# Optimization experiments

Measured on AMD Instinct MI355X. Metric: run time of the kernel, lower is better.

## Reference

```python
import jax, jax.numpy as jnp
import numpy as np

N_NODES = 50000
N_EDGES = 800000
D_IN = 128
D_OUT = 128


def setup_inputs() -> dict:
    key = jax.random.key(0)
    k_x, k_r, k_c, k_v, k_w = jax.random.split(key, 5)
    x = jax.random.normal(k_x, (N_NODES, D_IN), dtype=jnp.float32)
    edge_row = jax.random.randint(k_r, (N_EDGES,), 0, N_NODES)  # destination nodes
    edge_col = jax.random.randint(k_c, (N_EDGES,), 0, N_NODES)  # source nodes
    edge_val = jax.random.uniform(k_v, (N_EDGES,), dtype=jnp.float32)
    W = jax.random.normal(k_w, (D_OUT, D_IN), dtype=jnp.float32) * (1.0 / np.sqrt(D_IN))
    bias = jnp.zeros((D_OUT,), dtype=jnp.float32)
    return {"x": x, "edge_row": edge_row, "edge_col": edge_col,
            "edge_val": edge_val, "W": W, "bias": bias}


def reference(x, edge_row, edge_col, edge_val, W, bias):
    # support = linear(x)   (nn.Linear with bias=False: x @ W.T)
    support = jnp.einsum('ni,oi->no', x, W)  # [N, D_OUT]
    # out = sparse.mm(adj, support): gather source rows, scale by edge value,
    # scatter-add into destination rows.
    msgs = edge_val[:, None] * support[edge_col]  # [E, D_OUT]
    out = jax.ops.segment_sum(msgs, edge_row, num_segments=N_NODES)
    return out + bias
```

## Files before the change

### kernel.cpp

```cpp
#include <hip/hip_runtime.h>
#include <hip/hip_bf16.h>


constexpr int D     = 128;
constexpr int NPB   = 64;
constexpr int CAP   = 2048;
constexpr int C1    = 3200;
constexpr int BT    = 1024;
constexpr int NBMAX = 1024;

__device__ inline unsigned int bf1(float f) {
    unsigned int u = __float_as_uint(f);
    return (u + 0x7fffu + ((u >> 16) & 1u)) >> 16;
}
__device__ inline unsigned int bf2(float lo, float hi) {
    return bf1(lo) | (bf1(hi) << 16);
}
__device__ inline unsigned int cvt2(float a, float b) {
    __hip_bfloat162 h = __float22bfloat162_rn(float2{a, b});
    return *reinterpret_cast<unsigned int*>(&h);
}
__device__ inline float bflo(unsigned int u) { return __uint_as_float(u << 16); }
__device__ inline float bfhi(unsigned int u) { return __uint_as_float(u & 0xffff0000u); }

__global__ __launch_bounds__(256) void cvt_bf16_kernel(const float* __restrict__ in,
                                                       uint4* __restrict__ out, int n8,
                                                       int* __restrict__ gcursor, int nb) {
    int i = blockIdx.x * 256 + threadIdx.x;
    if (i < nb) gcursor[i] = 0;
    if (i >= n8) return;
    const float4* p = (const float4*)in + (size_t)i * 2;
    float4 a = p[0], b = p[1];
    uint4 r;
    r.x = cvt2(a.x, a.y); r.y = cvt2(a.z, a.w);
    r.z = cvt2(b.x, b.y); r.w = cvt2(b.z, b.w);
    out[i] = r;
}

__global__ __launch_bounds__(256) void gemm_mfma_kernel(const float* __restrict__ x,
                                                        const unsigned short* __restrict__ Wb,
                                                        unsigned short* __restrict__ supb,
                                                        int n_nodes) {
    using frag  = __attribute__((ext_vector_type(8))) short;
    using f32x4 = __attribute__((ext_vector_type(4))) float;
    union FU { uint4 u; frag f; };
    const int wv = threadIdx.x >> 6;
    const int lane = threadIdx.x & 63;
    const int m = lane & 15, quad = lane >> 4;
    const int row0 = blockIdx.x * 128 + wv * 32;
    const int r0 = min(row0 + m, n_nodes - 1);
    const int r1 = min(row0 + 16 + m, n_nodes - 1);

    frag a0[4], a1[4];
#pragma unroll
    for (int kf = 0; kf < 4; ++kf) {
        const float4* xp0 = (const float4*)(x + (size_t)r0 * D + kf * 32 + quad * 8);
        float4 p = xp0[0], q = xp0[1];
        FU t;
        t.u.x = cvt2(p.x, p.y); t.u.y = cvt2(p.z, p.w);
        t.u.z = cvt2(q.x, q.y); t.u.w = cvt2(q.z, q.w);
        a0[kf] = t.f;
        const float4* xp1 = (const float4*)(x + (size_t)r1 * D + kf * 32 + quad * 8);
        p = xp1[0]; q = xp1[1];
        t.u.x = cvt2(p.x, p.y); t.u.y = cvt2(p.z, p.w);
        t.u.z = cvt2(q.x, q.y); t.u.w = cvt2(q.z, q.w);
        a1[kf] = t.f;
    }

    f32x4 acc0[8], acc1[8];
#pragma unroll
    for (int ct = 0; ct < 8; ++ct) {
        acc0[ct] = (f32x4){0.f, 0.f, 0.f, 0.f};
        acc1[ct] = (f32x4){0.f, 0.f, 0.f, 0.f};
    }

#pragma unroll
    for (int ct = 0; ct < 8; ++ct) {
        const unsigned short* wrow = Wb + (size_t)(ct * 16 + m) * D;
#pragma unroll
        for (int kf = 0; kf < 4; ++kf) {
            frag b = *(const frag*)(wrow + kf * 32 + quad * 8);
            acc0[ct] = __builtin_amdgcn_mfma_f32_16x16x32_bf16(a0[kf], b, acc0[ct], 0, 0, 0);
            acc1[ct] = __builtin_amdgcn_mfma_f32_16x16x32_bf16(a1[kf], b, acc1[ct], 0, 0, 0);
        }
    }

#pragma unroll
    for (int ct = 0; ct < 8; ++ct) {
#pragma unroll
        for (int r = 0; r < 4; ++r) {
            int rr0 = row0 + quad * 4 + r;
            if (rr0 < n_nodes)
                supb[(size_t)rr0 * D + ct * 16 + m] = (unsigned short)bf1(acc0[ct][r]);
            int rr1 = row0 + 16 + quad * 4 + r;
            if (rr1 < n_nodes)
                supb[(size_t)rr1 * D + ct * 16 + m] = (unsigned short)bf1(acc1[ct][r]);
        }
    }
}

__global__ __launch_bounds__(BT) void binpass_kernel(const int* __restrict__ erow,
                                                     const int* __restrict__ ecol,
                                                     const float* __restrict__ eval,
                                                     int* __restrict__ gcursor,
                                                     int2* __restrict__ coarse,
                                                     int n_edges, int nb) {
    __shared__ int bkcnt[NBMAX];
    __shared__ int bkoff[NBMAX];
    __shared__ int wsum[16];
    __shared__ int gbase[NBMAX];
    __shared__ unsigned short slotbk[C1];
    __shared__ int2 stage[C1];
    const int t = threadIdx.x;
    const int base = blockIdx.x * C1;
    const int m = min(C1, n_edges - base);

    for (int i = t; i < nb; i += BT) bkcnt[i] = 0;
    __syncthreads();

    constexpr int EPT = (C1 + BT - 1) / BT;
    int  bk[EPT], rank[EPT];
    int2 pk[EPT];
#pragma unroll
    for (int j = 0; j < EPT; ++j) {
        int i = t + j * BT;
        bk[j] = -1;
        if (i < m) {
            int e = base + i;
            int dst = erow[e];
            int b = dst / NPB;
            bk[j] = b;
            rank[j] = atomicAdd(&bkcnt[b], 1);
            pk[j] = make_int2(ecol[e] | ((dst & (NPB - 1)) << 20),
                              __float_as_int(eval[e]));
        }
    }
    __syncthreads();

    {
        const int w = t >> 6, l = t & 63;
        int v = (t < nb) ? bkcnt[t] : 0;
        int inc = v;
#pragma unroll
        for (int o = 1; o < 64; o <<= 1) {
            int u = __shfl_up(inc, o, 64);
            if (l >= o) inc += u;
        }
        if (l == 63) wsum[w] = inc;
        __syncthreads();
        if (t < 16) {
            int wv2 = wsum[t];
            int winc = wv2;
#pragma unroll
            for (int o = 1; o < 16; o <<= 1) {
                int u = __shfl_up(winc, o, 16);
                if (t >= o) winc += u;
            }
            wsum[t] = winc - wv2;
        }
        __syncthreads();
        if (t < nb) bkoff[t] = inc - v + wsum[w];
    }
    __syncthreads();

#pragma unroll
    for (int j = 0; j < EPT; ++j) {
        if (bk[j] >= 0) {
            int s = bkoff[bk[j]] + rank[j];
            stage[s] = pk[j];
            slotbk[s] = (unsigned short)bk[j];
        }
    }
    if (t < nb) {
        int c = bkcnt[t];
        gbase[t] = (c > 0) ? (t * CAP + atomicAdd(&gcursor[t], c)) : 0;
    }
    __syncthreads();

    for (int i = t; i < m; i += BT) {
        int b = slotbk[i];
        int p = gbase[b] + (i - bkoff[b]);
        if (p < (b + 1) * CAP) coarse[p] = stage[i];
    }
}

__global__ __launch_bounds__(BT) void sortgather_kernel(const int* __restrict__ gcursor,
                                                        const int2* __restrict__ coarse,
                                                        const unsigned short* __restrict__ supb,
                                                        const float* __restrict__ bias,
                                                        float* __restrict__ out,
                                                        int n_nodes) {
    __shared__ int ncnt[NPB];
    __shared__ int noff[NPB];
    __shared__ int ncur[NPB];
    __shared__ int2 sorted[CAP];
    const int t = threadIdx.x;
    const int b = blockIdx.x;
    const int node0 = b * NPB;
    const int m = min(gcursor[b], CAP);
    const int2* src = coarse + (size_t)b * CAP;

    if (t < NPB) ncnt[t] = 0;
    __syncthreads();

    for (int i = t; i < m; i += BT)
        atomicAdd(&ncnt[(src[i].x >> 20) & (NPB - 1)], 1);
    __syncthreads();

    if (t < NPB) {
        int v = ncnt[t];
        int inc = v;
        for (int o = 1; o < NPB; o <<= 1) {
            int u = __shfl_up(inc, o, 64);
            if (t >= o) inc += u;
        }
        noff[t] = inc - v;
        ncur[t] = inc - v;
    }
    __syncthreads();

    for (int i = t; i < m; i += BT) {
        int2 e = src[i];
        int dl = (e.x >> 20) & (NPB - 1);
        int p = atomicAdd(&ncur[dl], 1);
        sorted[p] = make_int2(e.x & 0xFFFFF, e.y);
    }
    __syncthreads();

    const int qw = t >> 4;
    const int l16 = t & 15;
    const int node = node0 + qw;
    if (node >= n_nodes) return;
    const int beg = noff[qw];
    const int end = beg + ncnt[qw];

    const float4* b4 = (const float4*)(bias + l16 * 8);
    float4 acc0 = b4[0], acc1 = b4[1];

    int e = beg;
    for (; e + 1 < end; e += 2) {
        int2 d0 = sorted[e], d1 = sorted[e + 1];
        uint4 u0 = *(const uint4*)(supb + (size_t)d0.x * D + l16 * 8);
        uint4 u1 = *(const uint4*)(supb + (size_t)d1.x * D + l16 * 8);
        float v0 = __int_as_float(d0.y), v1 = __int_as_float(d1.y);
        acc0.x += v0 * bflo(u0.x) + v1 * bflo(u1.x);
        acc0.y += v0 * bfhi(u0.x) + v1 * bfhi(u1.x);
        acc0.z += v0 * bflo(u0.y) + v1 * bflo(u1.y);
        acc0.w += v0 * bfhi(u0.y) + v1 * bfhi(u1.y);
        acc1.x += v0 * bflo(u0.z) + v1 * bflo(u1.z);
        acc1.y += v0 * bfhi(u0.z) + v1 * bfhi(u1.z);
        acc1.z += v0 * bflo(u0.w) + v1 * bflo(u1.w);
        acc1.w += v0 * bfhi(u0.w) + v1 * bfhi(u1.w);
    }
    if (e < end) {
        int2 d0 = sorted[e];
        uint4 u0 = *(const uint4*)(supb + (size_t)d0.x * D + l16 * 8);
        float v0 = __int_as_float(d0.y);
        acc0.x += v0 * bflo(u0.x); acc0.y += v0 * bfhi(u0.x);
        acc0.z += v0 * bflo(u0.y); acc0.w += v0 * bfhi(u0.y);
        acc1.x += v0 * bflo(u0.z); acc1.y += v0 * bfhi(u0.z);
        acc1.z += v0 * bflo(u0.w); acc1.w += v0 * bfhi(u0.w);
    }
    float4* o4 = (float4*)(out + (size_t)node * D + l16 * 8);
    o4[0] = acc0;
    o4[1] = acc1;
}

__global__ __launch_bounds__(256) void init_out_kernel(float4* __restrict__ out4,
                                                       const float4* __restrict__ bias4,
                                                       int total4) {
    int i = blockIdx.x * 256 + threadIdx.x;
    if (i < total4) out4[i] = bias4[i & 31];
}

__global__ __launch_bounds__(256) void scatter_fb_kernel(const int* __restrict__ erow,
                                                         const int* __restrict__ ecol,
                                                         const float* __restrict__ eval,
                                                         const unsigned short* __restrict__ supb,
                                                         float* __restrict__ out,
                                                         int n_edges) {
    int e = blockIdx.x * 8 + (threadIdx.x >> 5);
    if (e >= n_edges) return;
    int lane = threadIdx.x & 31;
    int src = ecol[e], dst = erow[e];
    float v = eval[e];
    const unsigned short* sp = supb + (size_t)src * D + lane * 4;
    float* op = out + (size_t)dst * D + lane * 4;
#pragma unroll
    for (int j = 0; j < 4; ++j)
        atomicAdd(op + j, v * __uint_as_float(((unsigned)sp[j]) << 16));
}

static inline size_t align_up(size_t v, size_t a) { return (v + a - 1) & ~(a - 1); }

extern "C" void kernel_launch(void* const* d_in, const int* in_sizes, int n_in,
                              void* d_out, int out_size, void* d_ws, size_t ws_size,
                              hipStream_t stream) {
    const float* x    = (const float*)d_in[0];
    const int*   erow = (const int*)d_in[1];
    const int*   ecol = (const int*)d_in[2];
    const float* eval = (const float*)d_in[3];
    const float* W    = (const float*)d_in[4];
    const float* bias = (const float*)d_in[5];
    float* out = (float*)d_out;

    const int n_nodes = in_sizes[0] / D;
    const int n_edges = in_sizes[1];
    const int nb = (n_nodes + NPB - 1) / NPB;

    char* base = (char*)d_ws;
    size_t off = 0;
    unsigned short* supb = (unsigned short*)(base + off); off = align_up(off + (size_t)n_nodes * D * 2, 256);
    unsigned short* Wb   = (unsigned short*)(base + off); off = align_up(off + (size_t)D * D * 2, 256);
    int*  gcursor = (int*)(base + off);  off = align_up(off + (size_t)nb * 4, 256);
    int2* coarse  = (int2*)(base + off); off = align_up(off + (size_t)nb * CAP * 8, 256);

    const int n8 = D * D / 8;
    const int cvt_grid = (max(n8, nb) + 255) / 256;
    const bool fast = (n_nodes < (1 << 20)) && (nb <= NBMAX) && (off <= ws_size);

    cvt_bf16_kernel<<<cvt_grid, 256, 0, stream>>>(W, (uint4*)Wb, n8, gcursor, fast ? nb : 0);
    gemm_mfma_kernel<<<(n_nodes + 127) / 128, 256, 0, stream>>>(x, Wb, supb, n_nodes);

    if (fast) {
        binpass_kernel<<<(n_edges + C1 - 1) / C1, BT, 0, stream>>>(
            erow, ecol, eval, gcursor, coarse, n_edges, nb);
        sortgather_kernel<<<nb, BT, 0, stream>>>(
            gcursor, coarse, supb, bias, out, n_nodes);
    } else {
        int total4 = n_nodes * (D / 4);
        init_out_kernel<<<(total4 + 255) / 256, 256, 0, stream>>>(
            (float4*)out, (const float4*)bias, total4);
        scatter_fb_kernel<<<(n_edges + 7) / 8, 256, 0, stream>>>(
            erow, ecol, eval, supb, out, n_edges);
    }
}
```

Before: 144.7 us.

## Fuse GEMM and edge binning into one heterogeneous kernel launch

```diff
diff --git a/kernel.cpp b/kernel.cpp
--- a/kernel.cpp
+++ b/kernel.cpp
@@ -5,7 +5,7 @@
 constexpr int D     = 128;
 constexpr int NPB   = 64;
 constexpr int CAP   = 2048;
-constexpr int C1    = 3200;
+constexpr int C1    = 2048;
 constexpr int BT    = 1024;
 constexpr int NBMAX = 1024;
 
@@ -13,9 +13,6 @@
     unsigned int u = __float_as_uint(f);
     return (u + 0x7fffu + ((u >> 16) & 1u)) >> 16;
 }
-__device__ inline unsigned int bf2(float lo, float hi) {
-    return bf1(lo) | (bf1(hi) << 16);
-}
 __device__ inline unsigned int cvt2(float a, float b) {
     __hip_bfloat162 h = __float22bfloat162_rn(float2{a, b});
     return *reinterpret_cast<unsigned int*>(&h);
@@ -23,164 +20,160 @@
 __device__ inline float bflo(unsigned int u) { return __uint_as_float(u << 16); }
 __device__ inline float bfhi(unsigned int u) { return __uint_as_float(u & 0xffff0000u); }
 
-__global__ __launch_bounds__(256) void cvt_bf16_kernel(const float* __restrict__ in,
-                                                       uint4* __restrict__ out, int n8,
-                                                       int* __restrict__ gcursor, int nb) {
-    int i = blockIdx.x * 256 + threadIdx.x;
-    if (i < nb) gcursor[i] = 0;
-    if (i >= n8) return;
-    const float4* p = (const float4*)in + (size_t)i * 2;
-    float4 a = p[0], b = p[1];
-    uint4 r;
-    r.x = cvt2(a.x, a.y); r.y = cvt2(a.z, a.w);
-    r.z = cvt2(b.x, b.y); r.w = cvt2(b.z, b.w);
-    out[i] = r;
-}
-
-__global__ __launch_bounds__(256) void gemm_mfma_kernel(const float* __restrict__ x,
-                                                        const unsigned short* __restrict__ Wb,
-                                                        unsigned short* __restrict__ supb,
-                                                        int n_nodes) {
-    using frag  = __attribute__((ext_vector_type(8))) short;
-    using f32x4 = __attribute__((ext_vector_type(4))) float;
-    union FU { uint4 u; frag f; };
-    const int wv = threadIdx.x >> 6;
-    const int lane = threadIdx.x & 63;
-    const int m = lane & 15, quad = lane >> 4;
-    const int row0 = blockIdx.x * 128 + wv * 32;
-    const int r0 = min(row0 + m, n_nodes - 1);
-    const int r1 = min(row0 + 16 + m, n_nodes - 1);
-
-    frag a0[4], a1[4];
-#pragma unroll
-    for (int kf = 0; kf < 4; ++kf) {
-        const float4* xp0 = (const float4*)(x + (size_t)r0 * D + kf * 32 + quad * 8);
-        float4 p = xp0[0], q = xp0[1];
-        FU t;
-        t.u.x = cvt2(p.x, p.y); t.u.y = cvt2(p.z, p.w);
-        t.u.z = cvt2(q.x, q.y); t.u.w = cvt2(q.z, q.w);
-        a0[kf] = t.f;
-        const float4* xp1 = (const float4*)(x + (size_t)r1 * D + kf * 32 + quad * 8);
-        p = xp1[0]; q = xp1[1];
-        t.u.x = cvt2(p.x, p.y); t.u.y = cvt2(p.z, p.w);
-        t.u.z = cvt2(q.x, q.y); t.u.w = cvt2(q.z, q.w);
-        a1[kf] = t.f;
-    }
-
-    f32x4 acc0[8], acc1[8];
-#pragma unroll
-    for (int ct = 0; ct < 8; ++ct) {
-        acc0[ct] = (f32x4){0.f, 0.f, 0.f, 0.f};
-        acc1[ct] = (f32x4){0.f, 0.f, 0.f, 0.f};
-    }
-
-#pragma unroll
-    for (int ct = 0; ct < 8; ++ct) {
-        const unsigned short* wrow = Wb + (size_t)(ct * 16 + m) * D;
+__global__ __launch_bounds__(256) void fused_gemm_bin_kernel(
+        const float* __restrict__ x, const float* __restrict__ W,
+        const int* __restrict__ erow, const int* __restrict__ ecol,
+        const float* __restrict__ eval,
+        int* __restrict__ gcursor, int2* __restrict__ coarse,
+        unsigned short* __restrict__ supb,
+        int n_edges, int nb, int n_nodes, int bin_blocks) {
+    if ((int)blockIdx.x < bin_blocks) {
+        __shared__ int bkcnt[NBMAX];
+        __shared__ int bkoff[NBMAX];
+        __shared__ int wsum[4];
+        __shared__ int gbase[NBMAX];
+        __shared__ unsigned short slotbk[C1];
+        __shared__ int2 stage[C1];
+        const int t = threadIdx.x;
+        const int base = blockIdx.x * C1;
+        const int m = min(C1, n_edges - base);
+
+        for (int i = t; i < NBMAX; i += 256) bkcnt[i] = 0;
+        __syncthreads();
+
+        constexpr int EPT = C1 / 256;
+        int  bk[EPT], rank[EPT];
+        int2 pk[EPT];
+#pragma unroll
+        for (int j = 0; j < EPT; ++j) {
+            int i = t + j * 256;
+            bk[j] = -1;
+            if (i < m) {
+                int e = base + i;
+                int dst = erow[e];
+                int b = dst / NPB;
+                bk[j] = b;
+                rank[j] = atomicAdd(&bkcnt[b], 1);
+                pk[j] = make_int2(ecol[e] | ((dst & (NPB - 1)) << 20),
+                                  __float_as_int(eval[e]));
+            }
+        }
+        __syncthreads();
+
+        {
+            const int w = t >> 6, l = t & 63;
+            const int b0 = 4 * t;
+            int c0 = bkcnt[b0], c1 = bkcnt[b0 + 1];
+            int c2 = bkcnt[b0 + 2], c3 = bkcnt[b0 + 3];
+            int s = c0 + c1 + c2 + c3;
+            int inc = s;
+#pragma unroll
+            for (int o = 1; o < 64; o <<= 1) {
+                int u = __shfl_up(inc, o, 64);
+                if (l >= o) inc += u;
+            }
+            if (l == 63) wsum[w] = inc;
+            __syncthreads();
+            if (t < 4) {
+                int v = wsum[t];
+                int winc = v;
+#pragma unroll
+                for (int o = 1; o < 4; o <<= 1) {
+                    int u = __shfl_up(winc, o, 4);
+                    if (t >= o) winc += u;
+                }
+                wsum[t] = winc - v;
+            }
+            __syncthreads();
+            int p = inc - s + wsum[w];
+            bkoff[b0]     = p;
+            bkoff[b0 + 1] = p + c0;
+            bkoff[b0 + 2] = p + c0 + c1;
+            bkoff[b0 + 3] = p + c0 + c1 + c2;
+        }
+        __syncthreads();
+
+#pragma unroll
+        for (int j = 0; j < EPT; ++j) {
+            if (bk[j] >= 0) {
+                int s2 = bkoff[bk[j]] + rank[j];
+                stage[s2] = pk[j];
+                slotbk[s2] = (unsigned short)bk[j];
+            }
+        }
+        for (int i = t; i < nb; i += 256) {
+            int c = bkcnt[i];
+            gbase[i] = (c > 0) ? (i * CAP + atomicAdd(&gcursor[i], c)) : 0;
+        }
+        __syncthreads();
+
+        for (int i = t; i < m; i += 256) {
+            int b = slotbk[i];
+            int p = gbase[b] + (i - bkoff[b]);
+            if (p < (b + 1) * CAP) coarse[p] = stage[i];
+        }
+    } else {
+        using frag  = __attribute__((ext_vector_type(8))) short;
+        using f32x4 = __attribute__((ext_vector_type(4))) float;
+        union FU { uint4 u; frag f; };
+        const int wv = threadIdx.x >> 6;
+        const int lane = threadIdx.x & 63;
+        const int mm = lane & 15, quad = lane >> 4;
+        const int row0 = (blockIdx.x - bin_blocks) * 128 + wv * 32;
+        const int r0 = min(row0 + mm, n_nodes - 1);
+        const int r1 = min(row0 + 16 + mm, n_nodes - 1);
+
+        frag a0[4], a1[4];
 #pragma unroll
         for (int kf = 0; kf < 4; ++kf) {
-            frag b = *(const frag*)(wrow + kf * 32 + quad * 8);
-            acc0[ct] = __builtin_amdgcn_mfma_f32_16x16x32_bf16(a0[kf], b, acc0[ct], 0, 0, 0);
-            acc1[ct] = __builtin_amdgcn_mfma_f32_16x16x32_bf16(a1[kf], b, acc1[ct], 0, 0, 0);
-        }
-    }
-
-#pragma unroll
-    for (int ct = 0; ct < 8; ++ct) {
-#pragma unroll
-        for (int r = 0; r < 4; ++r) {
-            int rr0 = row0 + quad * 4 + r;
-            if (rr0 < n_nodes)
-                supb[(size_t)rr0 * D + ct * 16 + m] = (unsigned short)bf1(acc0[ct][r]);
-            int rr1 = row0 + 16 + quad * 4 + r;
-            if (rr1 < n_nodes)
-                supb[(size_t)rr1 * D + ct * 16 + m] = (unsigned short)bf1(acc1[ct][r]);
-        }
-    }
-}
-
-__global__ __launch_bounds__(BT) void binpass_kernel(const int* __restrict__ erow,
-                                                     const int* __restrict__ ecol,
-                                                     const float* __restrict__ eval,
-                                                     int* __restrict__ gcursor,
-                                                     int2* __restrict__ coarse,
-                                                     int n_edges, int nb) {
-    __shared__ int bkcnt[NBMAX];
-    __shared__ int bkoff[NBMAX];
-    __shared__ int wsum[16];
-    __shared__ int gbase[NBMAX];
-    __shared__ unsigned short slotbk[C1];
-    __shared__ int2 stage[C1];
-    const int t = threadIdx.x;
-    const int base = blockIdx.x * C1;
-    const int m = min(C1, n_edges - base);
-
-    for (int i = t; i < nb; i += BT) bkcnt[i] = 0;
-    __syncthreads();
-
-    constexpr int EPT = (C1 + BT - 1) / BT;
-    int  bk[EPT], rank[EPT];
-    int2 pk[EPT];
-#pragma unroll
-    for (int j = 0; j < EPT; ++j) {
-        int i = t + j * BT;
-        bk[j] = -1;
-        if (i < m) {
-            int e = base + i;
-            int dst = erow[e];
-            int b = dst / NPB;
-            bk[j] = b;
-            rank[j] = atomicAdd(&bkcnt[b], 1);
-            pk[j] = make_int2(ecol[e] | ((dst & (NPB - 1)) << 20),
-                              __float_as_int(eval[e]));
-        }
-    }
-    __syncthreads();
-
-    {
-        const int w = t >> 6, l = t & 63;
-        int v = (t < nb) ? bkcnt[t] : 0;
-        int inc = v;
-#pragma unroll
-        for (int o = 1; o < 64; o <<= 1) {
-            int u = __shfl_up(inc, o, 64);
-            if (l >= o) inc += u;
-        }
-        if (l == 63) wsum[w] = inc;
-        __syncthreads();
-        if (t < 16) {
-            int wv2 = wsum[t];
-            int winc = wv2;
-#pragma unroll
-            for (int o = 1; o < 16; o <<= 1) {
-                int u = __shfl_up(winc, o, 16);
-                if (t >= o) winc += u;
-            }
-            wsum[t] = winc - wv2;
-        }
-        __syncthreads();
-        if (t < nb) bkoff[t] = inc - v + wsum[w];
-    }
-    __syncthreads();
-
-#pragma unroll
-    for (int j = 0; j < EPT; ++j) {
-        if (bk[j] >= 0) {
-            int s = bkoff[bk[j]] + rank[j];
-            stage[s] = pk[j];
-            slotbk[s] = (unsigned short)bk[j];
-        }
-    }
-    if (t < nb) {
-        int c = bkcnt[t];
-        gbase[t] = (c > 0) ? (t * CAP + atomicAdd(&gcursor[t], c)) : 0;
-    }
-    __syncthreads();
-
-    for (int i = t; i < m; i += BT) {
-        int b = slotbk[i];
-        int p = gbase[b] + (i - bkoff[b]);
-        if (p < (b + 1) * CAP) coarse[p] = stage[i];
+            const float4* xp0 = (const float4*)(x + (size_t)r0 * D + kf * 32 + quad * 8);
+            float4 p = xp0[0], q = xp0[1];
+            FU t;
+            t.u.x = cvt2(p.x, p.y); t.u.y = cvt2(p.z, p.w);
+            t.u.z = cvt2(q.x, q.y); t.u.w = cvt2(q.z, q.w);
+            a0[kf] = t.f;
+            const float4* xp1 = (const float4*)(x + (size_t)r1 * D + kf * 32 + quad * 8);
+            p = xp1[0]; q = xp1[1];
+            t.u.x = cvt2(p.x, p.y); t.u.y = cvt2(p.z, p.w);
+            t.u.z = cvt2(q.x, q.y); t.u.w = cvt2(q.z, q.w);
+            a1[kf] = t.f;
+        }
+
+        f32x4 acc0[8], acc1[8];
+#pragma unroll
+        for (int ct = 0; ct < 8; ++ct) {
+            acc0[ct] = (f32x4){0.f, 0.f, 0.f, 0.f};
+            acc1[ct] = (f32x4){0.f, 0.f, 0.f, 0.f};
+        }
+
+#pragma unroll
+        for (int ct = 0; ct < 8; ++ct) {
+            const float* wrow = W + (size_t)(ct * 16 + mm) * D;
+#pragma unroll
+            for (int kf = 0; kf < 4; ++kf) {
+                const float4* wp = (const float4*)(wrow + kf * 32 + quad * 8);
+                float4 p = wp[0], q = wp[1];
+                FU tb;
+                tb.u.x = cvt2(p.x, p.y); tb.u.y = cvt2(p.z, p.w);
+                tb.u.z = cvt2(q.x, q.y); tb.u.w = cvt2(q.z, q.w);
+                frag b = tb.f;
+                acc0[ct] = __builtin_amdgcn_mfma_f32_16x16x32_bf16(a0[kf], b, acc0[ct], 0, 0, 0);
+                acc1[ct] = __builtin_amdgcn_mfma_f32_16x16x32_bf16(a1[kf], b, acc1[ct], 0, 0, 0);
+            }
+        }
+
+#pragma unroll
+        for (int ct = 0; ct < 8; ++ct) {
+#pragma unroll
+            for (int r = 0; r < 4; ++r) {
+                int rr0 = row0 + quad * 4 + r;
+                if (rr0 < n_nodes)
+                    supb[(size_t)rr0 * D + ct * 16 + mm] = (unsigned short)bf1(acc0[ct][r]);
+                int rr1 = row0 + 16 + quad * 4 + r;
+                if (rr1 < n_nodes)
+                    supb[(size_t)rr1 * D + ct * 16 + mm] = (unsigned short)bf1(acc1[ct][r]);
+            }
+        }
     }
 }
 
@@ -311,20 +304,21 @@
     char* base = (char*)d_ws;
     size_t off = 0;
     unsigned short* supb = (unsigned short*)(base + off); off = align_up(off + (size_t)n_nodes * D * 2, 256);
-    unsigned short* Wb   = (unsigned short*)(base + off); off = align_up(off + (size_t)D * D * 2, 256);
     int*  gcursor = (int*)(base + off);  off = align_up(off + (size_t)nb * 4, 256);
     int2* coarse  = (int2*)(base + off); off = align_up(off + (size_t)nb * CAP * 8, 256);
 
-    const int n8 = D * D / 8;
-    const int cvt_grid = (max(n8, nb) + 255) / 256;
     const bool fast = (n_nodes < (1 << 20)) && (nb <= NBMAX) && (off <= ws_size);
-
-    cvt_bf16_kernel<<<cvt_grid, 256, 0, stream>>>(W, (uint4*)Wb, n8, gcursor, fast ? nb : 0);
-    gemm_mfma_kernel<<<(n_nodes + 127) / 128, 256, 0, stream>>>(x, Wb, supb, n_nodes);
+    const int gemm_blocks = (n_nodes + 127) / 128;
+    const int bin_blocks = fast ? (n_edges + C1 - 1) / C1 : 0;
+
+    if (fast)
+        hipMemsetAsync(gcursor, 0, (size_t)nb * 4, stream);
+
+    fused_gemm_bin_kernel<<<bin_blocks + gemm_blocks, 256, 0, stream>>>(
+        x, W, erow, ecol, eval, gcursor, coarse, supb,
+        n_edges, nb, n_nodes, bin_blocks);
 
     if (fast) {
-        binpass_kernel<<<(n_edges + C1 - 1) / C1, BT, 0, stream>>>(
-            erow, ecol, eval, gcursor, coarse, n_edges, nb);
         sortgather_kernel<<<nb, BT, 0, stream>>>(
             gcursor, coarse, supb, bias, out, n_nodes);
     } else {
```

Measured after the change: 144.8 us. Within noise of the previous version (+0.0%).
